# Kernel tuning notes

Measured on AMD Instinct MI355X. Metric: run time of the kernel, lower is better.

Reference implementation:

```python
import jax, jax.numpy as jnp
import numpy as np

LOG2 = 0.6931471805599453

def logcosh(x):
    # numerically stable log(cosh(x)) = |x| + log1p(exp(-2|x|)) - log(2)
    ax = jnp.abs(x)
    return ax + jnp.log1p(jnp.exp(-2.0 * ax)) - LOG2

def setup_inputs() -> dict:
    key = jax.random.key(0)
    k1, k2, k3 = jax.random.split(key, 3)
    B, N, G, F = 16384, 1024, 256, 16  # batch, n_sites, n_symm, alpha_symm
    # each row of perms is a valid permutation of [0, N)
    perms = jax.vmap(lambda k: jax.random.permutation(k, N))(jax.random.split(k1, G)).astype(jnp.int32)
    x = jax.random.normal(k2, (B, N), dtype=jnp.float32)
    W = jax.random.normal(k3, (N, F), dtype=jnp.float32) * 0.1  # kernel_init = normal(0.1)
    b = jnp.zeros((F,), dtype=jnp.float32)
    v_bias = jnp.zeros((1,), dtype=jnp.float32)
    return {"x": x, "W": W, "b": b, "v_bias": v_bias, "perms": perms}

def reference(x, W, b, v_bias, perms):
    # scan over group permutations: gather x by perm, matmul, bias, logcosh, sum
    def f(carry, perm):
        y = x[..., perm] @ W + b          # [B, F]
        return carry + jnp.sum(logcosh(y), axis=-1), None
    y0 = jnp.zeros(x.shape[:-1], dtype=x.dtype)
    y_out, _ = jax.lax.scan(f, y0, perms)
    y_out = y_out + v_bias[0] * jnp.sum(x, axis=-1)
    return y_out
```

## Files before the change

### kernel.cpp

```cpp
#include <hip/hip_runtime.h>
#include <math.h>

typedef __bf16 bf16x8 __attribute__((ext_vector_type(8)));
typedef float f32x4 __attribute__((ext_vector_type(4)));


__device__ __forceinline__ unsigned short f2bf(float f) {
    unsigned int u = __float_as_uint(f);
    u += 0x7FFFu + ((u >> 16) & 1u);
    return (unsigned short)(u >> 16);
}

__device__ __forceinline__ float logcosh_fast(float v) {
    float a = fabsf(v);
    float t = __expf(-2.0f * a);
    return a + (__logf(1.0f + t) - 0.6931471805599453f);
}

template <int CTRL>
__device__ __forceinline__ float dppadd(float x) {
    int y = __builtin_amdgcn_update_dpp(0, __float_as_int(x), CTRL, 0xf, 0xf, true);
    return x + __int_as_float(y);
}

__device__ __forceinline__ void gload_lds16(const void* g, void* l) {
    __builtin_amdgcn_global_load_lds(
        (__attribute__((address_space(1))) void*)(void*)g,
        (__attribute__((address_space(3))) void*)l, 16, 0, 0);
}

__global__ __launch_bounds__(256) void k_invert(const int* __restrict__ perms,
                                                int* __restrict__ inv) {
    int t = blockIdx.x * 256 + threadIdx.x;
    int g = t >> 10, n = t & 1023;
    inv[(g << 10) + perms[t]] = n;
}

__global__ __launch_bounds__(256) void k_build_bt(const float* __restrict__ W,
                                                  const int* __restrict__ inv,
                                                  unsigned short* __restrict__ bT) {
    int j = blockIdx.x;
    int g = j >> 4, f = j & 15;
    const int* invg = inv + (g << 10);
    size_t rowbase = (size_t)j << 10;
#pragma unroll
    for (int i = 0; i < 4; ++i) {
        int k = (i << 8) + threadIdx.x;
        int n = invg[k];
        bT[rowbase + k] = f2bf(W[(n << 4) + f]);
    }
}

__global__ __launch_bounds__(256) void k_convert(const float* __restrict__ x,
                                                 const float* __restrict__ vb,
                                                 unsigned short* __restrict__ xb,
                                                 float* __restrict__ out) {
    int row = blockIdx.x, tid = threadIdx.x;
    size_t base = ((size_t)row << 10) + (tid << 2);
    float4 v = *reinterpret_cast<const float4*>(x + base);
    ushort4 h;
    h.x = f2bf(v.x); h.y = f2bf(v.y); h.z = f2bf(v.z); h.w = f2bf(v.w);
    *reinterpret_cast<ushort4*>(xb + base) = h;
    float s = v.x + v.y + v.z + v.w;
#pragma unroll
    for (int off = 32; off > 0; off >>= 1) s += __shfl_down(s, off);
    __shared__ float ls[4];
    if ((tid & 63) == 0) ls[tid >> 6] = s;
    __syncthreads();
    if (tid == 0) out[row] = vb[0] * (ls[0] + ls[1] + ls[2] + ls[3]);
}


#define MFMA_QUAD(MH, NH)                                                        \
    _Pragma("unroll") for (int m_ = 0; m_ < 4; ++m_)                             \
    _Pragma("unroll") for (int n_ = 0; n_ < 2; ++n_)                             \
    _Pragma("unroll") for (int kk_ = 0; kk_ < 2; ++kk_)                          \
        acc[(MH) * 4 + m_][(NH) * 2 + n_] =                                      \
            __builtin_amdgcn_mfma_f32_16x16x32_bf16(                             \
                aF[(MH) * 4 + m_][kk_], bF[(NH) * 2 + n_][kk_],                  \
                acc[(MH) * 4 + m_][(NH) * 2 + n_], 0, 0, 0);

__global__ __launch_bounds__(512) void k_gemm(const unsigned short* __restrict__ xb,
                                              const unsigned short* __restrict__ bT,
                                              const float* __restrict__ bias,
                                              float* __restrict__ partial, int B) {
    __shared__ unsigned short As[2][256 * 64];
    __shared__ unsigned short Bs[2][256 * 64];

    const int tid = threadIdx.x;
    const int lane = tid & 63;
    const int wv = tid >> 6;
    const int wm = wv >> 2;
    const int wn = wv & 3;
    const int lr = lane & 15;
    const int lk = lane >> 4;

    const int fid = blockIdx.y * gridDim.x + blockIdx.x;
    const int cpx = (gridDim.x * gridDim.y) >> 3;
    const int swz = (fid & 7) * cpx + (fid >> 3);
    const int cbx = swz & 15;
    const int row0 = (swz >> 4) << 8;
    const int j0 = cbx << 8;

    const unsigned short* xbase = xb + ((size_t)row0 << 10);
    const unsigned short* bbase = bT + ((size_t)j0 << 10);

    auto stage_half = [&](unsigned short* dst, const unsigned short* src, int h) {
#pragma unroll
        for (int j = 0; j < 2; ++j) {
            int c0 = (h * 128 + j * 64) * 8;
            int cc = c0 + tid;
            int r = cc >> 3;
            int cs = (cc & 7) ^ (r & 7);
            gload_lds16(src + (((size_t)r) << 10) + (cs << 3),
                        dst + ((c0 + wv * 64) << 3));
        }
    };
    auto stage_s = [&](int t, int s) {
        int tt = (s == 0) ? t + 1 : t + 2;
        if (tt >= 16) return;
        int p = tt & 1;
        int kt = tt << 6;
        if (s == 0)      stage_half(Bs[p], bbase + kt, 1);
        else if (s == 1) stage_half(As[p], xbase + kt, 0);
        else if (s == 2) stage_half(As[p], xbase + kt, 1);
        else             stage_half(Bs[p], bbase + kt, 0);
    };

    f32x4 acc[8][4];
#pragma unroll
    for (int m = 0; m < 8; ++m)
#pragma unroll
        for (int n = 0; n < 4; ++n)
            acc[m][n] = {0.f, 0.f, 0.f, 0.f};

    stage_half(As[0], xbase + 0, 0);
    stage_half(As[0], xbase + 0, 1);
    stage_half(Bs[0], bbase + 0, 0);
    stage_half(Bs[0], bbase + 0, 1);
    stage_half(As[1], xbase + 64, 0);
    stage_half(As[1], xbase + 64, 1);
    stage_half(Bs[1], bbase + 64, 0);
    asm volatile("s_waitcnt vmcnt(6)" ::: "memory");
    __builtin_amdgcn_s_barrier();

#pragma unroll 2
    for (int t = 0; t < 16; ++t) {
        const int p = t & 1;
        const unsigned short* Ap = As[p];
        const unsigned short* Bp = Bs[p];
        bf16x8 aF[8][2], bF[4][2];

        __builtin_amdgcn_sched_barrier(0);
#pragma unroll
        for (int m = 0; m < 8; ++m) {
            int r = wm * 128 + m * 16 + lr;
#pragma unroll
            for (int kk = 0; kk < 2; ++kk) {
                int pos = ((kk << 2) + lk) ^ (r & 7);
                aF[m][kk] = *reinterpret_cast<const bf16x8*>(Ap + (r << 6) + (pos << 3));
            }
        }
#pragma unroll
        for (int n = 0; n < 4; ++n) {
            int rb = wn * 64 + n * 16 + lr;
#pragma unroll
            for (int kk = 0; kk < 2; ++kk) {
                int pos = ((kk << 2) + lk) ^ (rb & 7);
                bF[n][kk] = *reinterpret_cast<const bf16x8*>(Bp + (rb << 6) + (pos << 3));
            }
        }
        stage_s(t, 0);
        asm volatile("s_waitcnt lgkmcnt(0)" ::: "memory");
        __builtin_amdgcn_sched_barrier(0);
        __builtin_amdgcn_s_setprio(1);
        MFMA_QUAD(0, 0)
        __builtin_amdgcn_s_setprio(0);
        __builtin_amdgcn_s_barrier();

        __builtin_amdgcn_sched_barrier(0);
        stage_s(t, 1);
        __builtin_amdgcn_s_barrier();
        __builtin_amdgcn_sched_barrier(0);
        __builtin_amdgcn_s_setprio(1);
        MFMA_QUAD(1, 0)
        __builtin_amdgcn_s_setprio(0);
        __builtin_amdgcn_s_barrier();

        __builtin_amdgcn_sched_barrier(0);
        stage_s(t, 2);
        __builtin_amdgcn_s_barrier();
        __builtin_amdgcn_sched_barrier(0);
        __builtin_amdgcn_s_setprio(1);
        MFMA_QUAD(0, 1)
        __builtin_amdgcn_s_setprio(0);
        __builtin_amdgcn_s_barrier();

        __builtin_amdgcn_sched_barrier(0);
        stage_s(t, 3);
        __builtin_amdgcn_s_barrier();
        __builtin_amdgcn_sched_barrier(0);
        __builtin_amdgcn_s_setprio(1);
        MFMA_QUAD(1, 1)
        __builtin_amdgcn_s_setprio(0);
        if (t < 14) {
            asm volatile("s_waitcnt vmcnt(6)" ::: "memory");
        } else if (t == 14) {
            asm volatile("s_waitcnt vmcnt(0)" ::: "memory");
        }
        __builtin_amdgcn_s_barrier();
    }

    float* rowsum = (float*)&As[0][0];
    const float bv = bias[lr];
#pragma unroll
    for (int m = 0; m < 8; ++m) {
#pragma unroll
        for (int r = 0; r < 4; ++r) {
            float s = 0.f;
#pragma unroll
            for (int n = 0; n < 4; ++n) s += logcosh_fast(acc[m][n][r] + bv);
            s = dppadd<0x111>(s);
            s = dppadd<0x112>(s);
            s = dppadd<0x114>(s);
            s = dppadd<0x118>(s);
            if (lr == 15)
                rowsum[wn * 256 + wm * 128 + m * 16 + lk * 4 + r] = s;
        }
    }
    __syncthreads();
    if (tid < 256) {
        float s = rowsum[tid] + rowsum[256 + tid] + rowsum[512 + tid] + rowsum[768 + tid];
        partial[(size_t)cbx * B + row0 + tid] = s;
    }
}

__global__ __launch_bounds__(256) void k_final(const float* __restrict__ partial,
                                               float* __restrict__ out, int ncb, int B) {
    int b = blockIdx.x * 256 + threadIdx.x;
    float s = out[b];
    for (int c = 0; c < ncb; ++c) s += partial[(size_t)c * B + b];
    out[b] = s;
}

extern "C" void kernel_launch(void* const* d_in, const int* in_sizes, int n_in,
                              void* d_out, int out_size, void* d_ws, size_t ws_size,
                              hipStream_t stream) {
    const float* x      = (const float*)d_in[0];
    const float* W      = (const float*)d_in[1];
    const float* bias   = (const float*)d_in[2];
    const float* v_bias = (const float*)d_in[3];
    const int*   perms  = (const int*)d_in[4];
    float* out = (float*)d_out;

    const int N  = 1024;
    const int B  = in_sizes[0] / N;
    const int G  = in_sizes[4] / N;
    const int GF = G * 16;
    const int NCB = GF / 256;

    char* w = (char*)d_ws;
    unsigned short* xb = (unsigned short*)w;
    unsigned short* bT = (unsigned short*)(w + (size_t)B * N * 2);
    int* inv = (int*)(w + (size_t)B * N * 2 + (size_t)GF * N * 2);
    float* partial = (float*)(w + (size_t)B * N * 2 + (size_t)GF * N * 2
                              + (size_t)G * N * 4);

    k_invert<<<G * N / 256, 256, 0, stream>>>(perms, inv);
    k_build_bt<<<GF, 256, 0, stream>>>(W, inv, bT);
    k_convert<<<B, 256, 0, stream>>>(x, v_bias, xb, out);
    k_gemm<<<dim3(NCB, B / 256), 512, 0, stream>>>(xb, bT, bias, partial, B);
    k_final<<<B / 256, 256, 0, stream>>>(partial, out, NCB, B);
}
```

Before: 196.7 us.

## Split LDS fragment loads across MFMA quadrants and deepen staging pipeline

Restructures the GEMM main loop so A/B fragment reads from LDS are split into two halves, each issued just before the MFMA quadrant that needs it, rather than loaded all at once at the top of each k-step. The global-to-LDS staging order is changed to a one-slot-earlier rotation with vmcnt(2) waits, and fragment offsets are precomputed from per-lane constants. The aim is to overlap LDS reads and global loads with MFMA work and reduce register pressure and stalls. It adds more barriers and relies on precise waitcnt accounting, which, if wrong, could introduce races.

```diff
diff --git a/kernel.cpp b/kernel.cpp
--- a/kernel.cpp
+++ b/kernel.cpp
@@ -28,6 +28,9 @@
         (__attribute__((address_space(1))) void*)(void*)g,
         (__attribute__((address_space(3))) void*)l, 16, 0, 0);
 }
+
+#define SBAR()  __builtin_amdgcn_s_barrier()
+#define SCHED() __builtin_amdgcn_sched_barrier(0)
 
 __global__ __launch_bounds__(256) void k_invert(const int* __restrict__ perms,
                                                 int* __restrict__ inv) {
@@ -105,6 +108,11 @@
     const unsigned short* xbase = xb + ((size_t)row0 << 10);
     const unsigned short* bbase = bT + ((size_t)j0 << 10);
 
+    const int aRow = (wm * 128 + lr) * 64;
+    const int bRow = (wn * 64 + lr) * 64;
+    const int po0 = (lk ^ (lr & 7)) * 8;
+    const int po1 = ((4 + lk) ^ (lr & 7)) * 8;
+
     auto stage_half = [&](unsigned short* dst, const unsigned short* src, int h) {
 #pragma unroll
         for (int j = 0; j < 2; ++j) {
@@ -116,15 +124,12 @@
                         dst + ((c0 + wv * 64) << 3));
         }
     };
-    auto stage_s = [&](int t, int s) {
-        int tt = (s == 0) ? t + 1 : t + 2;
-        if (tt >= 16) return;
-        int p = tt & 1;
-        int kt = tt << 6;
-        if (s == 0)      stage_half(Bs[p], bbase + kt, 1);
-        else if (s == 1) stage_half(As[p], xbase + kt, 0);
-        else if (s == 2) stage_half(As[p], xbase + kt, 1);
-        else             stage_half(Bs[p], bbase + kt, 0);
+    auto stage_slot = [&](int tile, int part) {
+        if (tile > 15) return;
+        int p = tile & 1;
+        const unsigned short* src = (part < 2 ? xbase : bbase) + (tile << 6);
+        unsigned short* dst = (part < 2 ? &As[p][0] : &Bs[p][0]);
+        stage_half(dst, src, part & 1);
     };
 
     f32x4 acc[8][4];
@@ -134,81 +139,88 @@
         for (int n = 0; n < 4; ++n)
             acc[m][n] = {0.f, 0.f, 0.f, 0.f};
 
-    stage_half(As[0], xbase + 0, 0);
-    stage_half(As[0], xbase + 0, 1);
-    stage_half(Bs[0], bbase + 0, 0);
-    stage_half(Bs[0], bbase + 0, 1);
-    stage_half(As[1], xbase + 64, 0);
-    stage_half(As[1], xbase + 64, 1);
-    stage_half(Bs[1], bbase + 64, 0);
-    asm volatile("s_waitcnt vmcnt(6)" ::: "memory");
-    __builtin_amdgcn_s_barrier();
-
-#pragma unroll 2
-    for (int t = 0; t < 16; ++t) {
-        const int p = t & 1;
-        const unsigned short* Ap = As[p];
-        const unsigned short* Bp = Bs[p];
-        bf16x8 aF[8][2], bF[4][2];
-
-        __builtin_amdgcn_sched_barrier(0);
-#pragma unroll
-        for (int m = 0; m < 8; ++m) {
-            int r = wm * 128 + m * 16 + lr;
-#pragma unroll
-            for (int kk = 0; kk < 2; ++kk) {
-                int pos = ((kk << 2) + lk) ^ (r & 7);
-                aF[m][kk] = *reinterpret_cast<const bf16x8*>(Ap + (r << 6) + (pos << 3));
-            }
-        }
-#pragma unroll
-        for (int n = 0; n < 4; ++n) {
-            int rb = wn * 64 + n * 16 + lr;
-#pragma unroll
-            for (int kk = 0; kk < 2; ++kk) {
-                int pos = ((kk << 2) + lk) ^ (rb & 7);
-                bF[n][kk] = *reinterpret_cast<const bf16x8*>(Bp + (rb << 6) + (pos << 3));
-            }
-        }
-        stage_s(t, 0);
-        asm volatile("s_waitcnt lgkmcnt(0)" ::: "memory");
-        __builtin_amdgcn_sched_barrier(0);
-        __builtin_amdgcn_s_setprio(1);
-        MFMA_QUAD(0, 0)
-        __builtin_amdgcn_s_setprio(0);
-        __builtin_amdgcn_s_barrier();
-
-        __builtin_amdgcn_sched_barrier(0);
-        stage_s(t, 1);
-        __builtin_amdgcn_s_barrier();
-        __builtin_amdgcn_sched_barrier(0);
-        __builtin_amdgcn_s_setprio(1);
-        MFMA_QUAD(1, 0)
-        __builtin_amdgcn_s_setprio(0);
-        __builtin_amdgcn_s_barrier();
-
-        __builtin_amdgcn_sched_barrier(0);
-        stage_s(t, 2);
-        __builtin_amdgcn_s_barrier();
-        __builtin_amdgcn_sched_barrier(0);
-        __builtin_amdgcn_s_setprio(1);
-        MFMA_QUAD(0, 1)
-        __builtin_amdgcn_s_setprio(0);
-        __builtin_amdgcn_s_barrier();
-
-        __builtin_amdgcn_sched_barrier(0);
-        stage_s(t, 3);
-        __builtin_amdgcn_s_barrier();
-        __builtin_amdgcn_sched_barrier(0);
-        __builtin_amdgcn_s_setprio(1);
-        MFMA_QUAD(1, 1)
-        __builtin_amdgcn_s_setprio(0);
-        if (t < 14) {
-            asm volatile("s_waitcnt vmcnt(6)" ::: "memory");
-        } else if (t == 14) {
-            asm volatile("s_waitcnt vmcnt(0)" ::: "memory");
-        }
-        __builtin_amdgcn_s_barrier();
+    stage_slot(0, 0); stage_slot(0, 1); stage_slot(0, 2); stage_slot(0, 3);
+    stage_slot(1, 0);
+    asm volatile("s_waitcnt vmcnt(2)" ::: "memory");
+    SCHED();
+    SBAR();
+
+    for (int tt = 0; tt < 8; ++tt) {
+        const int t = tt * 2;
+
+        auto half_iter = [&](const unsigned short* Ap, const unsigned short* Bp,
+                             int st1, int st4, int vm) {
+            bf16x8 aF[8][2], bF[4][2];
+
+#pragma unroll
+            for (int m = 0; m < 4; ++m) {
+                aF[m][0] = *reinterpret_cast<const bf16x8*>(Ap + aRow + po0 + m * 1024);
+                aF[m][1] = *reinterpret_cast<const bf16x8*>(Ap + aRow + po1 + m * 1024);
+            }
+#pragma unroll
+            for (int n = 0; n < 2; ++n) {
+                bF[n][0] = *reinterpret_cast<const bf16x8*>(Bp + bRow + po0 + n * 1024);
+                bF[n][1] = *reinterpret_cast<const bf16x8*>(Bp + bRow + po1 + n * 1024);
+            }
+            stage_slot(st1, 1);
+            SCHED();
+            SBAR();
+            asm volatile("s_waitcnt lgkmcnt(0)" ::: "memory");
+            SCHED();
+            __builtin_amdgcn_s_setprio(1);
+            MFMA_QUAD(0, 0)
+            __builtin_amdgcn_s_setprio(0);
+            SCHED();
+            SBAR();
+
+#pragma unroll
+            for (int m = 4; m < 8; ++m) {
+                aF[m][0] = *reinterpret_cast<const bf16x8*>(Ap + aRow + po0 + m * 1024);
+                aF[m][1] = *reinterpret_cast<const bf16x8*>(Ap + aRow + po1 + m * 1024);
+            }
+            SCHED();
+#pragma unroll
+            for (int n = 2; n < 4; ++n) {
+                bF[n][0] = *reinterpret_cast<const bf16x8*>(Bp + bRow + po0 + n * 1024);
+                bF[n][1] = *reinterpret_cast<const bf16x8*>(Bp + bRow + po1 + n * 1024);
+            }
+            stage_slot(st1, 2);
+            SCHED();
+            SBAR();
+            asm volatile("s_waitcnt lgkmcnt(4)" ::: "memory");
+            SCHED();
+            __builtin_amdgcn_s_setprio(1);
+            MFMA_QUAD(1, 0)
+            __builtin_amdgcn_s_setprio(0);
+            SCHED();
+            SBAR();
+
+            stage_slot(st1, 3);
+            SCHED();
+            SBAR();
+            asm volatile("s_waitcnt lgkmcnt(0)" ::: "memory");
+            SCHED();
+            __builtin_amdgcn_s_setprio(1);
+            MFMA_QUAD(0, 1)
+            __builtin_amdgcn_s_setprio(0);
+            SCHED();
+            SBAR();
+
+            stage_slot(st4, 0);
+            SCHED();
+            SBAR();
+            __builtin_amdgcn_s_setprio(1);
+            MFMA_QUAD(1, 1)
+            __builtin_amdgcn_s_setprio(0);
+            SCHED();
+            if (vm == 2)      { asm volatile("s_waitcnt vmcnt(2)" ::: "memory"); }
+            else if (vm == 0) { asm volatile("s_waitcnt vmcnt(0)" ::: "memory"); }
+            SCHED();
+            SBAR();
+        };
+
+        half_iter(As[0], Bs[0], t + 1, t + 2, (tt < 7) ? 2 : 0);
+        half_iter(As[1], Bs[1], t + 2, t + 3, (tt < 7) ? 2 : -1);
     }
 
     float* rowsum = (float*)&As[0][0];
```

Measured after the change: 204.4 us. 3.9% more time.
